# Kernel optimization log

Measured on AMD Instinct MI355X. Metric: run time of the kernel, lower is better.

Reference implementation:

```python
import jax, jax.numpy as jnp
import numpy as np

NUM_EXPERT = 16
D_MODEL = 1024
TOP_K = 2
N_TOKENS = 2048


def setup_inputs() -> dict:
    key = jax.random.key(0)
    k1, k2, k3, k4, k5 = jax.random.split(key, 5)
    inp = jax.random.normal(k1, (N_TOKENS, D_MODEL), dtype=jnp.float32)
    gate_idx = jax.random.randint(k2, (N_TOKENS, TOP_K), 0, NUM_EXPERT, dtype=jnp.int64)
    gate_score = jax.random.uniform(k3, (N_TOKENS, TOP_K), dtype=jnp.float32)
    # per-expert Linear(d_model, d_model) params (fan-in uniform init, like torch)
    bound = 1.0 / np.sqrt(D_MODEL)
    W = jax.random.uniform(k4, (NUM_EXPERT, D_MODEL, D_MODEL), dtype=jnp.float32,
                           minval=-bound, maxval=bound)
    b = jax.random.uniform(k5, (NUM_EXPERT, D_MODEL), dtype=jnp.float32,
                           minval=-bound, maxval=bound)
    return {"inp": inp, "gate_idx": gate_idx, "gate_score": gate_score, "W": W, "b": b}


def reference(inp, gate_idx, gate_score, W, b):
    T, d = inp.shape
    top_k = gate_idx.shape[1]
    # dispatch: repeat each token top_k times -> [T*top_k, d]
    x_rep = jnp.repeat(inp, top_k, axis=0)
    g = gate_idx.reshape(-1)  # [T*top_k]
    # brute-force: every expert applied to every dispatched token, then select
    # outs_all: [E, T*top_k, d]
    outs_all = jnp.einsum('td,edh->eth', x_rep, W) + b[:, None, :]
    expert_out = outs_all[g, jnp.arange(T * top_k)]  # [T*top_k, d]
    # weighted combine: bmm(gate_score[T,1,k], expert_out[T,k,d]) -> [T,d]
    y = jnp.einsum('tk,tkd->td', gate_score, expert_out.reshape(T, top_k, d))
    return y
```

## Files before the change

### kernel.cpp

```cpp
#include <hip/hip_runtime.h>
#include <hip/hip_bf16.h>

#define T_TOKENS 2048
#define DMODEL   1024
#define NEXPERT  16
#define TOPK     2
#define NASSIGN  (T_TOKENS * TOPK)

#define GBM 64
#define GBN 128
#define GBK 128

typedef __attribute__((ext_vector_type(8))) short  short8;
typedef __attribute__((ext_vector_type(4))) float  floatx4;
typedef __attribute__((ext_vector_type(8))) unsigned short ushort8;

__device__ __forceinline__ unsigned short f2bf(float f) {
    unsigned u = __builtin_bit_cast(unsigned, f);
    u += 0x7fff + ((u >> 16) & 1);
    return (unsigned short)(u >> 16);
}

__device__ __forceinline__ void g2l16(const void* g, void* l) {
    __builtin_amdgcn_global_load_lds(
        (__attribute__((address_space(1))) void*)g,
        (__attribute__((address_space(3))) void*)l, 16, 0, 0);
}

__global__ __launch_bounds__(256) void prep(
    const float* __restrict__ x,
    const int*   __restrict__ gate_idx,
    const float* __restrict__ W,
    unsigned short* __restrict__ xbf,
    unsigned short* __restrict__ wbf,
    int* __restrict__ counts, int* __restrict__ offsets, int* __restrict__ list)
{
    __shared__ __align__(16) unsigned short sT[64][72];
    const int bid = blockIdx.x;
    const int t   = threadIdx.x;

    if (bid == 0) {
        int* s_cnt = (int*)&sT[0][0];
        int* s_off = s_cnt + NEXPERT;
        if (t < NEXPERT) s_cnt[t] = 0;
        __syncthreads();
        for (int a = t; a < NASSIGN; a += 256)
            atomicAdd(&s_cnt[gate_idx[a]], 1);
        __syncthreads();
        if (t == 0) {
            int run = 0;
            for (int e = 0; e < NEXPERT; e++) { s_off[e] = run; run += s_cnt[e]; }
        }
        __syncthreads();
        if (t < NEXPERT) {
            counts[t]  = s_cnt[t];
            offsets[t] = s_off[t];
            s_cnt[t]   = s_off[t];
        }
        __syncthreads();
        for (int a = t; a < NASSIGN; a += 256) {
            int e = gate_idx[a];
            list[atomicAdd(&s_cnt[e], 1)] = a;
        }
    } else if (bid <= T_TOKENS / 2) {
        const int tr = (bid - 1) * 2 + (t >> 7);
        const int c  = (t & 127) * 8;
        const float4* p = (const float4*)(x + (size_t)tr * DMODEL + c);
        const float4 v0 = p[0], v1 = p[1];
        __align__(16) unsigned short cv[8];
        cv[0] = f2bf(v0.x); cv[1] = f2bf(v0.y); cv[2] = f2bf(v0.z); cv[3] = f2bf(v0.w);
        cv[4] = f2bf(v1.x); cv[5] = f2bf(v1.y); cv[6] = f2bf(v1.z); cv[7] = f2bf(v1.w);
        *(ushort8*)(xbf + (size_t)tr * DMODEL + c) = *(ushort8*)&cv[0];
    } else {
        const int wb = bid - (T_TOKENS / 2 + 1);
        const int e  = wb >> 8;
        const int k0 = ((wb >> 4) & 15) * 64;
        const int n0 = (wb & 15) * 64;
        const int ks = t >> 4;
        const int nq = (t & 15) * 4;
        const float* srcbase = W + ((size_t)(e * DMODEL + k0 + ks)) * DMODEL + n0 + nq;
        #pragma unroll
        for (int c = 0; c < 4; c++) {
            const int k = c * 16 + ks;
            const float4 v = *(const float4*)(srcbase + (size_t)c * 16 * DMODEL);
            sT[nq + 0][k] = f2bf(v.x);
            sT[nq + 1][k] = f2bf(v.y);
            sT[nq + 2][k] = f2bf(v.z);
            sT[nq + 3][k] = f2bf(v.w);
        }
        __syncthreads();
        const int nr = t >> 2, kc = t & 3;
        ushort8 v0 = *(const ushort8*)&sT[nr][kc * 16];
        ushort8 v1 = *(const ushort8*)&sT[nr][kc * 16 + 8];
        unsigned short* dst = wbf + (size_t)(e * DMODEL + n0 + nr) * DMODEL + k0 + kc * 16;
        *(ushort8*)dst       = v0;
        *(ushort8*)(dst + 8) = v1;
    }
}

__global__ __launch_bounds__(256) void moe_gemm_bf(
    const unsigned short* __restrict__ xbf,
    const unsigned short* __restrict__ wbf,
    const float* __restrict__ bias,
    const float* __restrict__ score,
    const int*   __restrict__ counts,
    const int*   __restrict__ offsets,
    const int*   __restrict__ list,
    float*       __restrict__ eo)
{
    const int e   = blockIdx.z;
    const int cnt = counts[e];
    const int m0  = blockIdx.y * GBM;
    if (m0 >= cnt) return;
    const int n0  = blockIdx.x * GBN;
    const int off = offsets[e];

    __shared__ __align__(16) unsigned short sA[GBM][GBK];
    __shared__ __align__(16) unsigned short sB[GBN][GBK];

    const int tid  = threadIdx.x;
    const int rsub = tid >> 4;
    const int pch  = tid & 15;

    const unsigned short* asrc[4];
    #pragma unroll
    for (int c = 0; c < 4; c++) {
        const int row = c * 16 + rsub;
        const int gm  = m0 + row;
        const int tok = (gm < cnt) ? (list[off + gm] >> 1) : 0;
        asrc[c] = xbf + (size_t)tok * DMODEL + (pch ^ (row & 15)) * 8;
    }
    const unsigned short* wbbase = wbf + (size_t)e * DMODEL * DMODEL;
    const unsigned short* bsrc[8];
    #pragma unroll
    for (int c = 0; c < 8; c++) {
        const int row = c * 16 + rsub;
        bsrc[c] = wbbase + (size_t)(n0 + row) * DMODEL + (pch ^ (row & 15)) * 8;
    }

    char* lA = (char*)&sA[0][0] + tid * 16;
    char* lB = (char*)&sB[0][0] + tid * 16;

    const int wave = tid >> 6;
    const int lane = tid & 63;
    const int wn   = wave * 32;
    const int fr   = lane & 15;
    const int quad = lane >> 4;

    floatx4 acc[4][2] = {};

    for (int k0 = 0; k0 < DMODEL; k0 += GBK) {
        #pragma unroll
        for (int c = 0; c < 4; c++)
            g2l16(asrc[c] + k0, lA + c * 4096);
        #pragma unroll
        for (int c = 0; c < 8; c++)
            g2l16(bsrc[c] + k0, lB + c * 4096);
        __syncthreads();

        #pragma unroll
        for (int kk = 0; kk < 4; kk++) {
            const int cc = (kk * 4 + quad) ^ fr;
            short8 af[4], bf[2];
            #pragma unroll
            for (int mi = 0; mi < 4; mi++)
                af[mi] = *(const short8*)&sA[mi * 16 + fr][cc * 8];
            #pragma unroll
            for (int ni = 0; ni < 2; ni++)
                bf[ni] = *(const short8*)&sB[wn + ni * 16 + fr][cc * 8];
            #pragma unroll
            for (int mi = 0; mi < 4; mi++)
                #pragma unroll
                for (int ni = 0; ni < 2; ni++)
                    acc[mi][ni] = __builtin_amdgcn_mfma_f32_16x16x32_bf16(
                        af[mi], bf[ni], acc[mi][ni], 0, 0, 0);
        }
        __syncthreads();
    }

    const int colA = n0 + wn + fr;
    const int colB = colA + 16;
    const float bv0 = bias[e * DMODEL + colA];
    const float bv1 = bias[e * DMODEL + colB];
    #pragma unroll
    for (int mi = 0; mi < 4; mi++) {
        const int rb = mi * 16 + quad * 4;
        #pragma unroll
        for (int r = 0; r < 4; r++) {
            const int gm = m0 + rb + r;
            if (gm >= cnt) continue;
            const int a = list[off + gm];
            const float s = score[a];
            float* row = eo + (size_t)a * DMODEL;
            row[colA] = s * (acc[mi][0][r] + bv0);
            row[colB] = s * (acc[mi][1][r] + bv1);
        }
    }
}

__global__ __launch_bounds__(256) void combine(const float* __restrict__ eo,
                                               float* __restrict__ out) {
    const int t = blockIdx.x;
    const int d = threadIdx.x * 4;
    const float4 a = *(const float4*)(eo + (size_t)(2 * t)     * DMODEL + d);
    const float4 b = *(const float4*)(eo + (size_t)(2 * t + 1) * DMODEL + d);
    *(float4*)(out + (size_t)t * DMODEL + d) =
        make_float4(a.x + b.x, a.y + b.y, a.z + b.z, a.w + b.w);
}

#define LDSK 72
__global__ __launch_bounds__(256) void moe_gemm_inline(
    const float* __restrict__ x, const float* __restrict__ W,
    const float* __restrict__ bias, const float* __restrict__ score,
    const int* __restrict__ counts, const int* __restrict__ offsets,
    const int* __restrict__ list, float* __restrict__ dst)
{
    const int e   = blockIdx.z;
    const int cnt = counts[e];
    const int m0  = blockIdx.y * 64;
    if (m0 >= cnt) return;
    const int n0  = blockIdx.x * 64;
    const int off = offsets[e];

    __shared__ __align__(16) unsigned short sA[64][LDSK];
    __shared__ __align__(16) unsigned short sB[64][LDSK];

    const int tid = threadIdx.x;
    const int arow = tid >> 2, aq = tid & 3, acol = aq * 16;
    const bool avalid = (m0 + arow) < cnt;
    int atok = 0;
    if (avalid) atok = list[off + m0 + arow] >> 1;
    const float* xsrc = x + (size_t)atok * DMODEL + acol;

    const int bk = tid >> 2, bng = tid & 3, bn = bng * 16, rot = tid & 15;
    const float* wsrc = W + (size_t)(e * DMODEL + bk) * DMODEL + n0 + bn;

    const int wave = tid >> 6, lane = tid & 63;
    const int wn = wave * 16, fr = lane & 15, quad = lane >> 4;

    floatx4 acc[4] = {};

    for (int k0 = 0; k0 < DMODEL; k0 += 64) {
        {
            float4 v[4];
            if (avalid) {
                const float4* p = (const float4*)(xsrc + k0);
                v[0] = p[0]; v[1] = p[1]; v[2] = p[2]; v[3] = p[3];
            } else {
                v[0] = v[1] = v[2] = v[3] = make_float4(0.f, 0.f, 0.f, 0.f);
            }
            __align__(16) unsigned short cvt[16];
            #pragma unroll
            for (int i = 0; i < 4; i++) {
                cvt[4*i+0] = f2bf(v[i].x); cvt[4*i+1] = f2bf(v[i].y);
                cvt[4*i+2] = f2bf(v[i].z); cvt[4*i+3] = f2bf(v[i].w);
            }
            *(ushort8*)&sA[arow][acol]     = *(ushort8*)&cvt[0];
            *(ushort8*)&sA[arow][acol + 8] = *(ushort8*)&cvt[8];
        }
        {
            const float4* p = (const float4*)(wsrc + (size_t)k0 * DMODEL);
            float4 v[4];
            v[0] = p[0]; v[1] = p[1]; v[2] = p[2]; v[3] = p[3];
            unsigned short cvt[16];
            #pragma unroll
            for (int i = 0; i < 4; i++) {
                cvt[4*i+0] = f2bf(v[i].x); cvt[4*i+1] = f2bf(v[i].y);
                cvt[4*i+2] = f2bf(v[i].z); cvt[4*i+3] = f2bf(v[i].w);
            }
            #pragma unroll
            for (int i = 0; i < 16; i++) {
                int m = (i + rot) & 15;
                sB[bn + m][bk] = cvt[m];
            }
        }
        __syncthreads();
        #pragma unroll
        for (int kk = 0; kk < 2; kk++) {
            const int ko = kk * 32 + quad * 8;
            short8 af[4], bf;
            #pragma unroll
            for (int mi = 0; mi < 4; mi++)
                af[mi] = *(const short8*)&sA[mi * 16 + fr][ko];
            bf = *(const short8*)&sB[wn + fr][ko];
            #pragma unroll
            for (int mi = 0; mi < 4; mi++)
                acc[mi] = __builtin_amdgcn_mfma_f32_16x16x32_bf16(af[mi], bf, acc[mi], 0, 0, 0);
        }
        __syncthreads();
    }

    const int col = n0 + wn + fr;
    const float bv = bias[e * DMODEL + col];
    #pragma unroll
    for (int mi = 0; mi < 4; mi++) {
        const int rb = mi * 16 + quad * 4;
        #pragma unroll
        for (int r = 0; r < 4; r++) {
            const int gm = m0 + rb + r;
            if (gm >= cnt) continue;
            const int a = list[off + gm];
            atomicAdd(&dst[(size_t)(a >> 1) * DMODEL + col],
                      score[a] * (acc[mi][r] + bv));
        }
    }
}

extern "C" void kernel_launch(void* const* d_in, const int* in_sizes, int n_in,
                              void* d_out, int out_size, void* d_ws, size_t ws_size,
                              hipStream_t stream) {
    const float* x    = (const float*)d_in[0];
    const int*   gidx = (const int*)d_in[1];
    const float* gsc  = (const float*)d_in[2];
    const float* W    = (const float*)d_in[3];
    const float* bias = (const float*)d_in[4];
    float* out = (float*)d_out;

    int* ws      = (int*)d_ws;
    int* counts  = ws;
    int* offsets = ws + 16;
    int* list    = ws + 32;

    const size_t eo_off  = 32 * 1024;
    const size_t eo_sz   = (size_t)NASSIGN * DMODEL * sizeof(float);
    const size_t xbf_off = eo_off + eo_sz;
    const size_t xbf_sz  = (size_t)T_TOKENS * DMODEL * sizeof(unsigned short);
    const size_t wbf_off = xbf_off + xbf_sz;
    const size_t wbf_sz  = (size_t)NEXPERT * DMODEL * DMODEL * sizeof(unsigned short);
    const size_t need_full = wbf_off + wbf_sz;

    float*          eo  = (float*)((char*)d_ws + eo_off);
    unsigned short* xbf = (unsigned short*)((char*)d_ws + xbf_off);
    unsigned short* wbf = (unsigned short*)((char*)d_ws + wbf_off);

    if (ws_size >= need_full) {
        prep<<<1 + T_TOKENS / 2 + NEXPERT * 16 * 16, 256, 0, stream>>>(
            x, gidx, W, xbf, wbf, counts, offsets, list);
        dim3 grid(DMODEL / GBN, 512 / GBM, NEXPERT);
        moe_gemm_bf<<<grid, 256, 0, stream>>>(xbf, wbf, bias, gsc,
                                              counts, offsets, list, eo);
        combine<<<T_TOKENS, 256, 0, stream>>>(eo, out);
    } else {
        prep<<<1, 256, 0, stream>>>(x, gidx, W, (unsigned short*)0, (unsigned short*)0,
                                    counts, offsets, list);
        hipMemsetAsync(d_out, 0, (size_t)T_TOKENS * DMODEL * sizeof(float), stream);
        dim3 grid(DMODEL / 64, 512 / 64, NEXPERT);
        moe_gemm_inline<<<grid, 256, 0, stream>>>(x, W, bias, gsc,
                                                  counts, offsets, list, out);
    }
}
```

Before: 150.0 us.

## Fuse prep, grouped GEMM and combine into one cooperative persistent kernel

```diff
diff --git a/kernel.cpp b/kernel.cpp
--- a/kernel.cpp
+++ b/kernel.cpp
@@ -1,5 +1,8 @@
 #include <hip/hip_runtime.h>
 #include <hip/hip_bf16.h>
+#include <hip/hip_cooperative_groups.h>
+
+namespace cg = cooperative_groups;
 
 #define T_TOKENS 2048
 #define DMODEL   1024
@@ -10,10 +13,12 @@
 #define GBM 64
 #define GBN 128
 #define GBK 128
+#define NBLK 512
 
 typedef __attribute__((ext_vector_type(8))) short  short8;
 typedef __attribute__((ext_vector_type(4))) float  floatx4;
 typedef __attribute__((ext_vector_type(8))) unsigned short ushort8;
+typedef __attribute__((ext_vector_type(4))) unsigned short usv4;
 
 __device__ __forceinline__ unsigned short f2bf(float f) {
     unsigned u = __builtin_bit_cast(unsigned, f);
@@ -27,25 +32,33 @@
         (__attribute__((address_space(3))) void*)l, 16, 0, 0);
 }
 
-__global__ __launch_bounds__(256) void prep(
+__global__ __launch_bounds__(256) void fused_moe(
     const float* __restrict__ x,
-    const int*   __restrict__ gate_idx,
+    const int*   __restrict__ gidx,
     const float* __restrict__ W,
+    const float* __restrict__ bias,
+    const float* __restrict__ score,
     unsigned short* __restrict__ xbf,
     unsigned short* __restrict__ wbf,
-    int* __restrict__ counts, int* __restrict__ offsets, int* __restrict__ list)
+    int* __restrict__ counts, int* __restrict__ offsets, int* __restrict__ list,
+    float* __restrict__ eo,
+    float* __restrict__ out)
 {
-    __shared__ __align__(16) unsigned short sT[64][72];
-    const int bid = blockIdx.x;
-    const int t   = threadIdx.x;
-
-    if (bid == 0) {
-        int* s_cnt = (int*)&sT[0][0];
-        int* s_off = s_cnt + NEXPERT;
+    __shared__ __align__(16) unsigned short sA[GBM][GBK];
+    __shared__ __align__(16) unsigned short sB[GBN][GBK];
+    __shared__ int rs[32];
+
+    const int b = blockIdx.x;
+    const int t = threadIdx.x;
+    cg::grid_group grid = cg::this_grid();
+
+    if (b == 0) {
+        int* s_cnt = rs;
+        int* s_off = rs + NEXPERT;
         if (t < NEXPERT) s_cnt[t] = 0;
         __syncthreads();
         for (int a = t; a < NASSIGN; a += 256)
-            atomicAdd(&s_cnt[gate_idx[a]], 1);
+            atomicAdd(&s_cnt[gidx[a]], 1);
         __syncthreads();
         if (t == 0) {
             int run = 0;
@@ -59,153 +72,182 @@
         }
         __syncthreads();
         for (int a = t; a < NASSIGN; a += 256) {
-            int e = gate_idx[a];
+            int e = gidx[a];
             list[atomicAdd(&s_cnt[e], 1)] = a;
         }
-    } else if (bid <= T_TOKENS / 2) {
-        const int tr = (bid - 1) * 2 + (t >> 7);
-        const int c  = (t & 127) * 8;
-        const float4* p = (const float4*)(x + (size_t)tr * DMODEL + c);
-        const float4 v0 = p[0], v1 = p[1];
-        __align__(16) unsigned short cv[8];
-        cv[0] = f2bf(v0.x); cv[1] = f2bf(v0.y); cv[2] = f2bf(v0.z); cv[3] = f2bf(v0.w);
-        cv[4] = f2bf(v1.x); cv[5] = f2bf(v1.y); cv[6] = f2bf(v1.z); cv[7] = f2bf(v1.w);
-        *(ushort8*)(xbf + (size_t)tr * DMODEL + c) = *(ushort8*)&cv[0];
-    } else {
-        const int wb = bid - (T_TOKENS / 2 + 1);
-        const int e  = wb >> 8;
-        const int k0 = ((wb >> 4) & 15) * 64;
-        const int n0 = (wb & 15) * 64;
+    }
+
+    #pragma unroll
+    for (int r = 0; r < 4; r++) {
+        const int row = b * 4 + r;
+        const float4 v = ((const float4*)(x + (size_t)row * DMODEL))[t];
+        usv4 c;
+        c.x = f2bf(v.x); c.y = f2bf(v.y); c.z = f2bf(v.z); c.w = f2bf(v.w);
+        ((usv4*)(xbf + (size_t)row * DMODEL))[t] = c;
+    }
+
+    {
+        unsigned short (*sT)[72] = (unsigned short (*)[72])&sA[0][0];
         const int ks = t >> 4;
         const int nq = (t & 15) * 4;
-        const float* srcbase = W + ((size_t)(e * DMODEL + k0 + ks)) * DMODEL + n0 + nq;
-        #pragma unroll
-        for (int c = 0; c < 4; c++) {
-            const int k = c * 16 + ks;
-            const float4 v = *(const float4*)(srcbase + (size_t)c * 16 * DMODEL);
-            sT[nq + 0][k] = f2bf(v.x);
-            sT[nq + 1][k] = f2bf(v.y);
-            sT[nq + 2][k] = f2bf(v.z);
-            sT[nq + 3][k] = f2bf(v.w);
-        }
-        __syncthreads();
         const int nr = t >> 2, kc = t & 3;
-        ushort8 v0 = *(const ushort8*)&sT[nr][kc * 16];
-        ushort8 v1 = *(const ushort8*)&sT[nr][kc * 16 + 8];
-        unsigned short* dst = wbf + (size_t)(e * DMODEL + n0 + nr) * DMODEL + k0 + kc * 16;
-        *(ushort8*)dst       = v0;
-        *(ushort8*)(dst + 8) = v1;
-    }
-}
-
-__global__ __launch_bounds__(256) void moe_gemm_bf(
-    const unsigned short* __restrict__ xbf,
-    const unsigned short* __restrict__ wbf,
-    const float* __restrict__ bias,
-    const float* __restrict__ score,
-    const int*   __restrict__ counts,
-    const int*   __restrict__ offsets,
-    const int*   __restrict__ list,
-    float*       __restrict__ eo)
-{
-    const int e   = blockIdx.z;
-    const int cnt = counts[e];
-    const int m0  = blockIdx.y * GBM;
-    if (m0 >= cnt) return;
-    const int n0  = blockIdx.x * GBN;
-    const int off = offsets[e];
-
-    __shared__ __align__(16) unsigned short sA[GBM][GBK];
-    __shared__ __align__(16) unsigned short sB[GBN][GBK];
-
-    const int tid  = threadIdx.x;
-    const int rsub = tid >> 4;
-    const int pch  = tid & 15;
-
-    const unsigned short* asrc[4];
+        for (int i = 0; i < 8; i++) {
+            const int idx = b * 8 + i;
+            const int e  = idx >> 8;
+            const int k0 = ((idx >> 4) & 15) * 64;
+            const int n0 = (idx & 15) * 64;
+            const float* srcbase = W + ((size_t)(e * DMODEL + k0 + ks)) * DMODEL + n0 + nq;
+            __syncthreads();
+            #pragma unroll
+            for (int c = 0; c < 4; c++) {
+                const int k = c * 16 + ks;
+                const float4 v = *(const float4*)(srcbase + (size_t)c * 16 * DMODEL);
+                sT[nq + 0][k] = f2bf(v.x);
+                sT[nq + 1][k] = f2bf(v.y);
+                sT[nq + 2][k] = f2bf(v.z);
+                sT[nq + 3][k] = f2bf(v.w);
+            }
+            __syncthreads();
+            ushort8 v0 = *(const ushort8*)&sT[nr][kc * 16];
+            ushort8 v1 = *(const ushort8*)&sT[nr][kc * 16 + 8];
+            unsigned short* dst = wbf + (size_t)(e * DMODEL + n0 + nr) * DMODEL + k0 + kc * 16;
+            *(ushort8*)dst       = v0;
+            *(ushort8*)(dst + 8) = v1;
+        }
+    }
+
+    grid.sync();
+
+    {
+        const int rsub = t >> 4;
+        const int pch  = t & 15;
+        const int wave = t >> 6;
+        const int lane = t & 63;
+        const int wn   = wave * 32;
+        const int fr   = lane & 15;
+        const int quad = lane >> 4;
+        char* lA = (char*)&sA[0][0] + t * 16;
+        char* lB = (char*)&sB[0][0] + t * 16;
+
+        for (int item = b; item < 1024; item += NBLK) {
+            const int e  = item >> 6;
+            const int mt = (item >> 3) & 7;
+            const int nt = item & 7;
+            const int cnt = counts[e];
+            const int m0  = mt * GBM;
+            if (m0 >= cnt) continue;
+            const int n0  = nt * GBN;
+            const int off = offsets[e];
+
+            const unsigned short* asrc[4];
+            #pragma unroll
+            for (int c = 0; c < 4; c++) {
+                const int row = c * 16 + rsub;
+                const int gm  = m0 + row;
+                const int tok = (gm < cnt) ? (list[off + gm] >> 1) : 0;
+                asrc[c] = xbf + (size_t)tok * DMODEL + (pch ^ (row & 15)) * 8;
+            }
+            const unsigned short* wbbase = wbf + (size_t)e * DMODEL * DMODEL;
+            const unsigned short* bsrc[8];
+            #pragma unroll
+            for (int c = 0; c < 8; c++) {
+                const int row = c * 16 + rsub;
+                bsrc[c] = wbbase + (size_t)(n0 + row) * DMODEL + (pch ^ (row & 15)) * 8;
+            }
+
+            floatx4 acc[4][2] = {};
+
+            for (int k0 = 0; k0 < DMODEL; k0 += GBK) {
+                __syncthreads();
+                #pragma unroll
+                for (int c = 0; c < 4; c++)
+                    g2l16(asrc[c] + k0, lA + c * 4096);
+                #pragma unroll
+                for (int c = 0; c < 8; c++)
+                    g2l16(bsrc[c] + k0, lB + c * 4096);
+                __syncthreads();
+
+                #pragma unroll
+                for (int kk = 0; kk < 4; kk++) {
+                    const int cc = (kk * 4 + quad) ^ fr;
+                    short8 af[4], bf[2];
+                    #pragma unroll
+                    for (int mi = 0; mi < 4; mi++)
+                        af[mi] = *(const short8*)&sA[mi * 16 + fr][cc * 8];
+                    #pragma unroll
+                    for (int ni = 0; ni < 2; ni++)
+                        bf[ni] = *(const short8*)&sB[wn + ni * 16 + fr][cc * 8];
+                    #pragma unroll
+                    for (int mi = 0; mi < 4; mi++)
+                        #pragma unroll
+                        for (int ni = 0; ni < 2; ni++)
+                            acc[mi][ni] = __builtin_amdgcn_mfma_f32_16x16x32_bf16(
+                                af[mi], bf[ni], acc[mi][ni], 0, 0, 0);
+                }
+            }
+            __syncthreads();
+
+            const int colA = n0 + wn + fr;
+            const int colB = colA + 16;
+            const float bv0 = bias[e * DMODEL + colA];
+            const float bv1 = bias[e * DMODEL + colB];
+            #pragma unroll
+            for (int mi = 0; mi < 4; mi++) {
+                const int rb = mi * 16 + quad * 4;
+                #pragma unroll
+                for (int r = 0; r < 4; r++) {
+                    const int gm = m0 + rb + r;
+                    if (gm >= cnt) continue;
+                    const int a = list[off + gm];
+                    const float s = score[a];
+                    float* row = eo + (size_t)a * DMODEL;
+                    row[colA] = s * (acc[mi][0][r] + bv0);
+                    row[colB] = s * (acc[mi][1][r] + bv1);
+                }
+            }
+        }
+    }
+
+    grid.sync();
+
     #pragma unroll
-    for (int c = 0; c < 4; c++) {
-        const int row = c * 16 + rsub;
-        const int gm  = m0 + row;
-        const int tok = (gm < cnt) ? (list[off + gm] >> 1) : 0;
-        asrc[c] = xbf + (size_t)tok * DMODEL + (pch ^ (row & 15)) * 8;
-    }
-    const unsigned short* wbbase = wbf + (size_t)e * DMODEL * DMODEL;
-    const unsigned short* bsrc[8];
-    #pragma unroll
-    for (int c = 0; c < 8; c++) {
-        const int row = c * 16 + rsub;
-        bsrc[c] = wbbase + (size_t)(n0 + row) * DMODEL + (pch ^ (row & 15)) * 8;
-    }
-
-    char* lA = (char*)&sA[0][0] + tid * 16;
-    char* lB = (char*)&sB[0][0] + tid * 16;
-
-    const int wave = tid >> 6;
-    const int lane = tid & 63;
-    const int wn   = wave * 32;
-    const int fr   = lane & 15;
-    const int quad = lane >> 4;
-
-    floatx4 acc[4][2] = {};
-
-    for (int k0 = 0; k0 < DMODEL; k0 += GBK) {
-        #pragma unroll
-        for (int c = 0; c < 4; c++)
-            g2l16(asrc[c] + k0, lA + c * 4096);
-        #pragma unroll
-        for (int c = 0; c < 8; c++)
-            g2l16(bsrc[c] + k0, lB + c * 4096);
-        __syncthreads();
-
-        #pragma unroll
-        for (int kk = 0; kk < 4; kk++) {
-            const int cc = (kk * 4 + quad) ^ fr;
-            short8 af[4], bf[2];
-            #pragma unroll
-            for (int mi = 0; mi < 4; mi++)
-                af[mi] = *(const short8*)&sA[mi * 16 + fr][cc * 8];
-            #pragma unroll
-            for (int ni = 0; ni < 2; ni++)
-                bf[ni] = *(const short8*)&sB[wn + ni * 16 + fr][cc * 8];
-            #pragma unroll
-            for (int mi = 0; mi < 4; mi++)
-                #pragma unroll
-                for (int ni = 0; ni < 2; ni++)
-                    acc[mi][ni] = __builtin_amdgcn_mfma_f32_16x16x32_bf16(
-                        af[mi], bf[ni], acc[mi][ni], 0, 0, 0);
-        }
-        __syncthreads();
-    }
-
-    const int colA = n0 + wn + fr;
-    const int colB = colA + 16;
-    const float bv0 = bias[e * DMODEL + colA];
-    const float bv1 = bias[e * DMODEL + colB];
-    #pragma unroll
-    for (int mi = 0; mi < 4; mi++) {
-        const int rb = mi * 16 + quad * 4;
-        #pragma unroll
-        for (int r = 0; r < 4; r++) {
-            const int gm = m0 + rb + r;
-            if (gm >= cnt) continue;
-            const int a = list[off + gm];
-            const float s = score[a];
-            float* row = eo + (size_t)a * DMODEL;
-            row[colA] = s * (acc[mi][0][r] + bv0);
-            row[colB] = s * (acc[mi][1][r] + bv1);
-        }
-    }
-}
-
-__global__ __launch_bounds__(256) void combine(const float* __restrict__ eo,
-                                               float* __restrict__ out) {
-    const int t = blockIdx.x;
-    const int d = threadIdx.x * 4;
-    const float4 a = *(const float4*)(eo + (size_t)(2 * t)     * DMODEL + d);
-    const float4 b = *(const float4*)(eo + (size_t)(2 * t + 1) * DMODEL + d);
-    *(float4*)(out + (size_t)t * DMODEL + d) =
-        make_float4(a.x + b.x, a.y + b.y, a.z + b.z, a.w + b.w);
+    for (int r = 0; r < 4; r++) {
+        const int tok = b * 4 + r;
+        const float4 a = ((const float4*)(eo + (size_t)(2 * tok)     * DMODEL))[t];
+        const float4 c = ((const float4*)(eo + (size_t)(2 * tok + 1) * DMODEL))[t];
+        ((float4*)(out + (size_t)tok * DMODEL))[t] =
+            make_float4(a.x + c.x, a.y + c.y, a.z + c.z, a.w + c.w);
+    }
+}
+
+__global__ void build_routing(const int* __restrict__ gate_idx,
+                              int* __restrict__ counts,
+                              int* __restrict__ offsets,
+                              int* __restrict__ list) {
+    __shared__ int s_cnt[NEXPERT];
+    __shared__ int s_off[NEXPERT];
+    const int tid = threadIdx.x;
+    if (tid < NEXPERT) s_cnt[tid] = 0;
+    __syncthreads();
+    for (int a = tid; a < NASSIGN; a += blockDim.x)
+        atomicAdd(&s_cnt[gate_idx[a]], 1);
+    __syncthreads();
+    if (tid == 0) {
+        int run = 0;
+        for (int e = 0; e < NEXPERT; e++) { s_off[e] = run; run += s_cnt[e]; }
+    }
+    __syncthreads();
+    if (tid < NEXPERT) {
+        counts[tid]  = s_cnt[tid];
+        offsets[tid] = s_off[tid];
+        s_cnt[tid]   = s_off[tid];
+    }
+    __syncthreads();
+    for (int a = tid; a < NASSIGN; a += blockDim.x) {
+        int e = gate_idx[a];
+        int pos = atomicAdd(&s_cnt[e], 1);
+        list[pos] = a;
+    }
 }
 
 #define LDSK 72
@@ -334,15 +376,14 @@
     unsigned short* wbf = (unsigned short*)((char*)d_ws + wbf_off);
 
     if (ws_size >= need_full) {
-        prep<<<1 + T_TOKENS / 2 + NEXPERT * 16 * 16, 256, 0, stream>>>(
-            x, gidx, W, xbf, wbf, counts, offsets, list);
-        dim3 grid(DMODEL / GBN, 512 / GBM, NEXPERT);
-        moe_gemm_bf<<<grid, 256, 0, stream>>>(xbf, wbf, bias, gsc,
-                                              counts, offsets, list, eo);
-        combine<<<T_TOKENS, 256, 0, stream>>>(eo, out);
+        void* args[] = { (void*)&x, (void*)&gidx, (void*)&W, (void*)&bias,
+                         (void*)&gsc, (void*)&xbf, (void*)&wbf,
+                         (void*)&counts, (void*)&offsets, (void*)&list,
+                         (void*)&eo, (void*)&out };
+        hipLaunchCooperativeKernel((void*)fused_moe, dim3(NBLK), dim3(256),
+                                   args, 0, stream);
     } else {
-        prep<<<1, 256, 0, stream>>>(x, gidx, W, (unsigned short*)0, (unsigned short*)0,
-                                    counts, offsets, list);
+        build_routing<<<1, 256, 0, stream>>>(gidx, counts, offsets, list);
         hipMemsetAsync(d_out, 0, (size_t)T_TOKENS * DMODEL * sizeof(float), stream);
         dim3 grid(DMODEL / 64, 512 / 64, NEXPERT);
         moe_gemm_inline<<<grid, 256, 0, stream>>>(x, W, bias, gsc,
```

After: 304.4 us. 2.03x slower.
